# Performance work log

Hardware: AMD Instinct MI355X
Metric: run time of the kernel (lower is better)

The kernel has to match this reference:

```python
import jax, jax.numpy as jnp
import numpy as np

N_LAYER = 2


def setup_inputs() -> dict:
    key = jax.random.key(0)
    k1, k2, k3, k4, k5 = jax.random.split(key, 5)
    N, E, D, C = 50000, 800000, 128, 40
    features = jax.random.normal(k1, (N, D), dtype=jnp.float32)
    adj_row = jax.random.randint(k2, (E,), 0, N, dtype=jnp.int32)
    adj_col = jax.random.randint(k3, (E,), 0, N, dtype=jnp.int32)
    adj_values = jax.random.uniform(k4, (E,), dtype=jnp.float32)
    lin = jax.random.normal(k5, (D, C), dtype=jnp.float32) * (1.0 / np.sqrt(D))
    return {"features": features, "adj_row": adj_row, "adj_col": adj_col,
            "adj_values": adj_values, "lin": lin}


def reference(features, adj_row, adj_col, adj_values, lin):
    N = features.shape[0]
    loop = jnp.arange(N, dtype=adj_row.dtype)
    # preprocess_adj: add self-loops, symmetric GCN normalization D^-1/2 (A+I) D^-1/2
    row = jnp.concatenate([adj_row, loop])
    col = jnp.concatenate([adj_col, loop])
    val = jnp.concatenate([adj_values, jnp.ones((N,), features.dtype)])
    deg = jax.ops.segment_sum(val, row, num_segments=N)
    dinv = jnp.where(deg > 0, jax.lax.rsqrt(jnp.maximum(deg, 1e-12)), 0.0)
    nval = dinv[row] * val * dinv[col]  # normalized edge weights [E+N]
    X = features
    layerwise = []
    for _ in range(N_LAYER):  # X = A_hat @ X (SpMM via gather + segment_sum)
        X = jax.ops.segment_sum(nval[:, None] * X[col], row, num_segments=N)
        layerwise.append(X)
    logits = X @ lin  # [N, out_dim]
    return (jax.nn.log_softmax(logits, axis=1), logits, tuple(layerwise))
```

## Files before the change

kernel.cpp:

```cpp
#include <hip/hip_runtime.h>
#include <math.h>

#define D_FEAT 128
#define SCAN_B 256
#define C_MAX  40
#define FIXP   33554432.0f


__device__ __forceinline__ unsigned bf16_rne(float x) {
    unsigned u = __float_as_uint(x);
    return (u + 0x7fffu + ((u >> 16) & 1u)) >> 16;
}
__device__ __forceinline__ unsigned pack2(float x, float y) {
    return bf16_rne(x) | (bf16_rne(y) << 16);
}
__device__ __forceinline__ float lo_f(unsigned g) { return __uint_as_float(g << 16); }
__device__ __forceinline__ float hi_f(unsigned g) { return __uint_as_float(g & 0xffff0000u); }


__global__ void k_init(unsigned long long* __restrict__ deg64, int N) {
    int i = blockIdx.x * blockDim.x + threadIdx.x;
    if (i < N) deg64[i] = (unsigned long long)(1.0f * FIXP);
}

__global__ void k_deg_hist(const int* __restrict__ row, const float* __restrict__ val,
                           unsigned long long* __restrict__ deg64,
                           int* __restrict__ rank, int E) {
    int e = blockIdx.x * blockDim.x + threadIdx.x;
    if (e >= E) return;
    int r = row[e];
    unsigned long long add = (1ull << 40) |
                             (unsigned long long)(val[e] * FIXP + 0.5f);
    unsigned long long old = atomicAdd(&deg64[r], add);
    rank[e] = (int)(old >> 40);
}


__global__ __launch_bounds__(SCAN_B) void k_part_sum(const unsigned long long* __restrict__ deg64,
                                                     int* __restrict__ part,
                                                     float* __restrict__ dinv,
                                                     int* __restrict__ cnt32, int N) {
    __shared__ int s[SCAN_B];
    int i = blockIdx.x * SCAN_B + threadIdx.x;
    int c = 0;
    if (i < N) {
        unsigned long long p = deg64[i];
        int cntv = (int)(p >> 40);
        float deg = (float)(p & ((1ull << 40) - 1)) * (1.0f / FIXP);
        dinv[i] = rsqrtf(fmaxf(deg, 1e-12f));
        c = (cntv + 7) & ~7;
        cnt32[i] = c;
    }
    s[threadIdx.x] = c;
    __syncthreads();
    for (int off = SCAN_B / 2; off; off >>= 1) {
        if (threadIdx.x < off) s[threadIdx.x] += s[threadIdx.x + off];
        __syncthreads();
    }
    if (threadIdx.x == 0) part[blockIdx.x] = s[0];
}

__global__ __launch_bounds__(SCAN_B) void k_part_scan(int* __restrict__ part, int nchunks,
                                                      int* __restrict__ rowptr, int N) {
    __shared__ int s[SCAN_B];
    int t = threadIdx.x;
    int v = (t < nchunks) ? part[t] : 0;
    s[t] = v;
    __syncthreads();
    for (int off = 1; off < SCAN_B; off <<= 1) {
        int add = (t >= off) ? s[t - off] : 0;
        __syncthreads();
        s[t] += add;
        __syncthreads();
    }
    if (t < nchunks) part[t] = s[t] - v;
    if (t == nchunks - 1) rowptr[N] = s[t];
}

__global__ __launch_bounds__(SCAN_B) void k_chunk_scan(const int* __restrict__ cnt32,
                                                       const int* __restrict__ part,
                                                       int* __restrict__ rowptr, int N) {
    __shared__ int s[SCAN_B];
    int t = threadIdx.x;
    int i = blockIdx.x * SCAN_B + t;
    int v = (i < N) ? cnt32[i] : 0;
    s[t] = v;
    __syncthreads();
    for (int off = 1; off < SCAN_B; off <<= 1) {
        int add = (t >= off) ? s[t - off] : 0;
        __syncthreads();
        s[t] += add;
        __syncthreads();
    }
    if (i < N) rowptr[i] = part[blockIdx.x] + s[t] - v;
}

__global__ void k_convert(const float* __restrict__ X, const float* __restrict__ dinv,
                          unsigned* __restrict__ Xb, int N) {
    int t = blockIdx.x * blockDim.x + threadIdx.x;
    if (t >= N * (D_FEAT / 8)) return;
    float w = dinv[t >> 4];
    float4 a = ((const float4*)X)[t * 2];
    float4 b = ((const float4*)X)[t * 2 + 1];
    uint4 o;
    o.x = pack2(w * a.x, w * a.y); o.y = pack2(w * a.z, w * a.w);
    o.z = pack2(w * b.x, w * b.y); o.w = pack2(w * b.z, w * b.w);
    ((uint4*)Xb)[t] = o;
}

__global__ void k_scatter(const int* __restrict__ row, const int* __restrict__ col,
                          const float* __restrict__ val, const int* __restrict__ rank,
                          const int* __restrict__ rowptr, int2* __restrict__ csr, int E) {
    int e = blockIdx.x * blockDim.x + threadIdx.x;
    if (e >= E) return;
    int r = row[e];
    int pos = rowptr[r] + rank[e];
    csr[pos] = make_int2(col[e] << 8, __float_as_int(val[e]));
}


__device__ __forceinline__ float2 spmm_row_bf16(const int* __restrict__ rowptr,
                                                const int2* __restrict__ csr,
                                                const char* __restrict__ XbB,
                                                int rowi, int lane) {
    const unsigned lane4 = (unsigned)lane << 2;
    unsigned gs = *(const unsigned*)(XbB + ((unsigned)rowi << 8) + lane4);
    float2 a0 = make_float2(lo_f(gs), hi_f(gs));
    float2 a1 = make_float2(0.f, 0.f), a2 = make_float2(0.f, 0.f), a3 = make_float2(0.f, 0.f);
    int e  = rowptr[rowi];
    int e1 = rowptr[rowi + 1];

    for (; e + 16 <= e1; e += 16) {
        const int4* cp = (const int4*)(csr + e);
        int4 q0 = cp[0], q1 = cp[1], q2 = cp[2], q3 = cp[3];
        int4 q4 = cp[4], q5 = cp[5], q6 = cp[6], q7 = cp[7];
        unsigned g0 = *(const unsigned*)(XbB + (unsigned)q0.x + lane4);
        unsigned g1 = *(const unsigned*)(XbB + (unsigned)q0.z + lane4);
        unsigned g2 = *(const unsigned*)(XbB + (unsigned)q1.x + lane4);
        unsigned g3 = *(const unsigned*)(XbB + (unsigned)q1.z + lane4);
        unsigned g4 = *(const unsigned*)(XbB + (unsigned)q2.x + lane4);
        unsigned g5 = *(const unsigned*)(XbB + (unsigned)q2.z + lane4);
        unsigned g6 = *(const unsigned*)(XbB + (unsigned)q3.x + lane4);
        unsigned g7 = *(const unsigned*)(XbB + (unsigned)q3.z + lane4);
        unsigned g8 = *(const unsigned*)(XbB + (unsigned)q4.x + lane4);
        unsigned g9 = *(const unsigned*)(XbB + (unsigned)q4.z + lane4);
        unsigned ga = *(const unsigned*)(XbB + (unsigned)q5.x + lane4);
        unsigned gb = *(const unsigned*)(XbB + (unsigned)q5.z + lane4);
        unsigned gc = *(const unsigned*)(XbB + (unsigned)q6.x + lane4);
        unsigned gd = *(const unsigned*)(XbB + (unsigned)q6.z + lane4);
        unsigned ge = *(const unsigned*)(XbB + (unsigned)q7.x + lane4);
        unsigned gf = *(const unsigned*)(XbB + (unsigned)q7.z + lane4);
        float w0 = __int_as_float(q0.y), w1 = __int_as_float(q0.w);
        float w2 = __int_as_float(q1.y), w3 = __int_as_float(q1.w);
        float w4 = __int_as_float(q2.y), w5 = __int_as_float(q2.w);
        float w6 = __int_as_float(q3.y), w7 = __int_as_float(q3.w);
        float w8 = __int_as_float(q4.y), w9 = __int_as_float(q4.w);
        float wa = __int_as_float(q5.y), wb = __int_as_float(q5.w);
        float wc = __int_as_float(q6.y), wd = __int_as_float(q6.w);
        float we = __int_as_float(q7.y), wf = __int_as_float(q7.w);
        a0.x += w0 * lo_f(g0); a0.y += w0 * hi_f(g0);
        a1.x += w1 * lo_f(g1); a1.y += w1 * hi_f(g1);
        a2.x += w2 * lo_f(g2); a2.y += w2 * hi_f(g2);
        a3.x += w3 * lo_f(g3); a3.y += w3 * hi_f(g3);
        a0.x += w4 * lo_f(g4); a0.y += w4 * hi_f(g4);
        a1.x += w5 * lo_f(g5); a1.y += w5 * hi_f(g5);
        a2.x += w6 * lo_f(g6); a2.y += w6 * hi_f(g6);
        a3.x += w7 * lo_f(g7); a3.y += w7 * hi_f(g7);
        a0.x += w8 * lo_f(g8); a0.y += w8 * hi_f(g8);
        a1.x += w9 * lo_f(g9); a1.y += w9 * hi_f(g9);
        a2.x += wa * lo_f(ga); a2.y += wa * hi_f(ga);
        a3.x += wb * lo_f(gb); a3.y += wb * hi_f(gb);
        a0.x += wc * lo_f(gc); a0.y += wc * hi_f(gc);
        a1.x += wd * lo_f(gd); a1.y += wd * hi_f(gd);
        a2.x += we * lo_f(ge); a2.y += we * hi_f(ge);
        a3.x += wf * lo_f(gf); a3.y += wf * hi_f(gf);
    }
    if (e < e1) {
        const int4* cp = (const int4*)(csr + e);
        int4 q0 = cp[0], q1 = cp[1], q2 = cp[2], q3 = cp[3];
        unsigned g0 = *(const unsigned*)(XbB + (unsigned)q0.x + lane4);
        unsigned g1 = *(const unsigned*)(XbB + (unsigned)q0.z + lane4);
        unsigned g2 = *(const unsigned*)(XbB + (unsigned)q1.x + lane4);
        unsigned g3 = *(const unsigned*)(XbB + (unsigned)q1.z + lane4);
        unsigned g4 = *(const unsigned*)(XbB + (unsigned)q2.x + lane4);
        unsigned g5 = *(const unsigned*)(XbB + (unsigned)q2.z + lane4);
        unsigned g6 = *(const unsigned*)(XbB + (unsigned)q3.x + lane4);
        unsigned g7 = *(const unsigned*)(XbB + (unsigned)q3.z + lane4);
        float w0 = __int_as_float(q0.y), w1 = __int_as_float(q0.w);
        float w2 = __int_as_float(q1.y), w3 = __int_as_float(q1.w);
        float w4 = __int_as_float(q2.y), w5 = __int_as_float(q2.w);
        float w6 = __int_as_float(q3.y), w7 = __int_as_float(q3.w);
        a0.x += w0 * lo_f(g0); a0.y += w0 * hi_f(g0);
        a1.x += w1 * lo_f(g1); a1.y += w1 * hi_f(g1);
        a2.x += w2 * lo_f(g2); a2.y += w2 * hi_f(g2);
        a3.x += w3 * lo_f(g3); a3.y += w3 * hi_f(g3);
        a0.x += w4 * lo_f(g4); a0.y += w4 * hi_f(g4);
        a1.x += w5 * lo_f(g5); a1.y += w5 * hi_f(g5);
        a2.x += w6 * lo_f(g6); a2.y += w6 * hi_f(g6);
        a3.x += w7 * lo_f(g7); a3.y += w7 * hi_f(g7);
    }
    float2 acc;
    acc.x = (a0.x + a1.x) + (a2.x + a3.x);
    acc.y = (a0.y + a1.y) + (a2.y + a3.y);
    return acc;
}


__global__ __launch_bounds__(256) void k_spmm_l1(const int* __restrict__ rowptr,
                                                 const int2* __restrict__ csr,
                                                 const float* __restrict__ dinv,
                                                 const unsigned* __restrict__ Xb,
                                                 float* __restrict__ Xout,
                                                 unsigned* __restrict__ XbOut, int N) {
    int lane = threadIdx.x & 63;
    int wid  = threadIdx.x >> 6;
    int rowi = blockIdx.x * 4 + wid;
    if (rowi >= N) return;
    float2 acc = spmm_row_bf16(rowptr, csr, (const char*)Xb, rowi, lane);
    float dr = dinv[rowi];
    float2 x1 = make_float2(dr * acc.x, dr * acc.y);
    ((float2*)Xout)[(size_t)rowi * 64 + lane] = x1;
    XbOut[((unsigned)rowi << 6) | lane] = pack2(dr * x1.x, dr * x1.y);
}

__global__ __launch_bounds__(256) void k_spmm_l2_head(const int* __restrict__ rowptr,
                                                      const int2* __restrict__ csr,
                                                      const float* __restrict__ dinv,
                                                      const unsigned* __restrict__ Xb,
                                                      float* __restrict__ Xout,
                                                      const float* __restrict__ lin,
                                                      float* __restrict__ lsm,
                                                      float* __restrict__ logits,
                                                      int N, int C) {
    __shared__ float lin_s[D_FEAT * C_MAX];
    __shared__ float xs[4][D_FEAT];
    int lane = threadIdx.x & 63;
    int wid  = threadIdx.x >> 6;
    int rowi = blockIdx.x * 4 + wid;

    for (int i = threadIdx.x; i < D_FEAT * C; i += 256) lin_s[i] = lin[i];

    float2 x2 = make_float2(0.f, 0.f);
    if (rowi < N) {
        float2 acc = spmm_row_bf16(rowptr, csr, (const char*)Xb, rowi, lane);
        float dr = dinv[rowi];
        x2 = make_float2(dr * acc.x, dr * acc.y);
        ((float2*)Xout)[(size_t)rowi * 64 + lane] = x2;
        xs[wid][2 * lane]     = x2.x;
        xs[wid][2 * lane + 1] = x2.y;
    }
    __syncthreads();
    if (rowi >= N) return;

    float a = 0.0f;
    if (lane < C) {
#pragma unroll 8
        for (int d = 0; d < D_FEAT; ++d)
            a += xs[wid][d] * lin_s[d * C + lane];
    }
    float m = (lane < C) ? a : -INFINITY;
    for (int off = 32; off; off >>= 1) m = fmaxf(m, __shfl_xor(m, off));
    float ev = (lane < C) ? __expf(a - m) : 0.0f;
    float s = ev;
    for (int off = 32; off; off >>= 1) s += __shfl_xor(s, off);
    float lse = m + logf(s);
    if (lane < C) {
        logits[(size_t)rowi * C + lane] = a;
        lsm[(size_t)rowi * C + lane]    = a - lse;
    }
}


__global__ __launch_bounds__(256) void k_spmm_f32(const int* __restrict__ rowptr,
                                                  const int2* __restrict__ csr,
                                                  const float* __restrict__ dinv,
                                                  const float* __restrict__ Xin,
                                                  float* __restrict__ Xout, int N) {
    int lane = threadIdx.x & 63;
    int wid  = threadIdx.x >> 6;
    int rowi = blockIdx.x * 4 + wid;
    if (rowi >= N) return;
    const float2* Xin2 = (const float2*)Xin;
    float dr = dinv[rowi];
    float2 v0 = Xin2[(size_t)rowi * 64 + lane];
    float2 a0 = make_float2(dr * v0.x, dr * v0.y);
    float2 a1 = make_float2(0.f, 0.f);
    int e  = rowptr[rowi];
    int e1 = rowptr[rowi + 1];
    for (; e < e1; e += 2) {
        int2 q0 = csr[e], q1 = csr[e + 1];
        unsigned c0 = (unsigned)q0.x >> 8, c1 = (unsigned)q1.x >> 8;
        float w0 = __int_as_float(q0.y) * dinv[c0];
        float w1 = __int_as_float(q1.y) * dinv[c1];
        float2 g0 = Xin2[(size_t)c0 * 64 + lane];
        float2 g1 = Xin2[(size_t)c1 * 64 + lane];
        a0.x += w0 * g0.x; a0.y += w0 * g0.y;
        a1.x += w1 * g1.x; a1.y += w1 * g1.y;
    }
    float2 acc = make_float2(dr * (a0.x + a1.x), dr * (a0.y + a1.y));
    ((float2*)Xout)[(size_t)rowi * 64 + lane] = acc;
}

__global__ __launch_bounds__(256) void k_head(const float* __restrict__ X,
                                              const float* __restrict__ lin,
                                              float* __restrict__ lsm,
                                              float* __restrict__ logits,
                                              int N, int C) {
    __shared__ float xs[4][D_FEAT];
    int lane = threadIdx.x & 63;
    int wid  = threadIdx.x >> 6;
    int node = blockIdx.x * 4 + wid;
    if (node < N) {
        xs[wid][lane]      = X[(size_t)node * D_FEAT + lane];
        xs[wid][lane + 64] = X[(size_t)node * D_FEAT + 64 + lane];
    }
    __syncthreads();
    if (node >= N) return;

    float acc = 0.0f;
    if (lane < C) {
        for (int d = 0; d < D_FEAT; ++d)
            acc += xs[wid][d] * lin[d * C + lane];
    }
    float m = (lane < C) ? acc : -INFINITY;
    for (int off = 32; off; off >>= 1) m = fmaxf(m, __shfl_xor(m, off));
    float ev = (lane < C) ? __expf(acc - m) : 0.0f;
    float s = ev;
    for (int off = 32; off; off >>= 1) s += __shfl_xor(s, off);
    float lse = m + logf(s);
    if (lane < C) {
        logits[(size_t)node * C + lane] = acc;
        lsm[(size_t)node * C + lane]    = acc - lse;
    }
}


extern "C" void kernel_launch(void* const* d_in, const int* in_sizes, int n_in,
                              void* d_out, int out_size, void* d_ws, size_t ws_size,
                              hipStream_t stream) {
    const float* features = (const float*)d_in[0];
    const int*   adj_row  = (const int*)d_in[1];
    const int*   adj_col  = (const int*)d_in[2];
    const float* adj_val  = (const float*)d_in[3];
    const float* lin      = (const float*)d_in[4];

    const int N = in_sizes[0] / D_FEAT;
    const int E = in_sizes[1];
    const int C = in_sizes[4] / D_FEAT;
    const int csrTot = E + 8 * N;

    float* out = (float*)d_out;
    const size_t NC = (size_t)N * C;
    const size_t ND = (size_t)N * D_FEAT;
    float* lsm    = out;
    float* logits = out + NC;
    float* X1     = out + 2 * NC;
    float* X2     = out + 2 * NC + ND;

    char* wp = (char*)d_ws;
    auto alloc = [&](size_t bytes) { char* p = wp; wp += (bytes + 15) & ~(size_t)15; return p; };
    unsigned long long* deg64 = (unsigned long long*)alloc((size_t)N * 8);
    float*    dinv   = (float*)alloc((size_t)N * 4);
    int*      cnt32  = (int*)alloc((size_t)N * 4);
    int*      rowptr = (int*)alloc((size_t)(N + 1) * 4);
    int*      part   = (int*)alloc(256 * 4);
    int*      rank   = (int*)alloc((size_t)E * 4);
    int2*     csr    = (int2*)alloc((size_t)csrTot * 8);
    unsigned* Xb0    = (unsigned*)alloc((size_t)N * (D_FEAT / 2) * 4);
    unsigned* Xb1    = (unsigned*)alloc((size_t)N * (D_FEAT / 2) * 4);

    const bool bf16_ok = ((size_t)(wp - (char*)d_ws) <= ws_size) && (C <= C_MAX);

    const int B = 256;
    const int nchunks = (N + SCAN_B - 1) / SCAN_B;

    hipMemsetAsync(csr, 0, (size_t)csrTot * 8, stream);
    k_init<<<(N + B - 1) / B, B, 0, stream>>>(deg64, N);
    k_deg_hist<<<(E + B - 1) / B, B, 0, stream>>>(adj_row, adj_val, deg64, rank, E);
    k_part_sum<<<nchunks, SCAN_B, 0, stream>>>(deg64, part, dinv, cnt32, N);
    k_part_scan<<<1, SCAN_B, 0, stream>>>(part, nchunks, rowptr, N);
    k_chunk_scan<<<nchunks, SCAN_B, 0, stream>>>(cnt32, part, rowptr, N);
    k_scatter<<<(E + B - 1) / B, B, 0, stream>>>(adj_row, adj_col, adj_val, rank,
                                                 rowptr, csr, E);

    int spmmBlocks = (N + 3) / 4;
    if (bf16_ok) {
        k_convert<<<(N * (D_FEAT / 8) + B - 1) / B, B, 0, stream>>>(features, dinv, Xb0, N);
        k_spmm_l1<<<spmmBlocks, 256, 0, stream>>>(rowptr, csr, dinv, Xb0, X1, Xb1, N);
        k_spmm_l2_head<<<spmmBlocks, 256, 0, stream>>>(rowptr, csr, dinv, Xb1, X2,
                                                       lin, lsm, logits, N, C);
    } else {
        k_spmm_f32<<<spmmBlocks, 256, 0, stream>>>(rowptr, csr, dinv, features, X1, N);
        k_spmm_f32<<<spmmBlocks, 256, 0, stream>>>(rowptr, csr, dinv, X1, X2, N);
        k_head<<<(N + 3) / 4, 256, 0, stream>>>(X2, lin, lsm, logits, N, C);
    }
}
```

Measured before the change: 181.7 us.

## Fuse three-pass scan into decoupled-lookback scan and merge scatter with convert

Replaces the partial-sum, partition-scan and chunk-scan kernels with a single kernel that uses a ticket-ordered decoupled lookback to build rowptr. The full CSR memset is dropped; only the padding slots of each row are zeroed inside the scan kernel. The edge scatter and the bf16 feature conversion are merged into one launch. This cuts several kernel launches and a large memset, at the cost of serialized spin-waits on chunk state across blocks.

```diff
diff --git a/kernel.cpp b/kernel.cpp
--- a/kernel.cpp
+++ b/kernel.cpp
@@ -6,6 +6,9 @@
 #define C_MAX  40
 #define FIXP   33554432.0f
 
+#define FLAG_AGG (1ull << 32)
+#define FLAG_INC (2ull << 32)
+
 
 __device__ __forceinline__ unsigned bf16_rne(float x) {
     unsigned u = __float_as_uint(x);
@@ -18,9 +21,14 @@
 __device__ __forceinline__ float hi_f(unsigned g) { return __uint_as_float(g & 0xffff0000u); }
 
 
-__global__ void k_init(unsigned long long* __restrict__ deg64, int N) {
+__global__ void k_init(unsigned long long* __restrict__ deg64,
+                       unsigned* __restrict__ ticket,
+                       unsigned long long* __restrict__ chunkState,
+                       int N, int nchunks) {
     int i = blockIdx.x * blockDim.x + threadIdx.x;
     if (i < N) deg64[i] = (unsigned long long)(1.0f * FIXP);
+    if (i < nchunks) chunkState[i] = 0ull;
+    if (i == 0) *ticket = 0u;
 }
 
 __global__ void k_deg_hist(const int* __restrict__ row, const float* __restrict__ val,
@@ -36,36 +44,30 @@
 }
 
 
-__global__ __launch_bounds__(SCAN_B) void k_part_sum(const unsigned long long* __restrict__ deg64,
-                                                     int* __restrict__ part,
+__global__ __launch_bounds__(SCAN_B) void k_scan_all(const unsigned long long* __restrict__ deg64,
                                                      float* __restrict__ dinv,
-                                                     int* __restrict__ cnt32, int N) {
+                                                     int* __restrict__ rowptr,
+                                                     int2* __restrict__ csr,
+                                                     unsigned* __restrict__ ticket,
+                                                     unsigned long long* __restrict__ chunkState,
+                                                     int N, int nchunks) {
     __shared__ int s[SCAN_B];
-    int i = blockIdx.x * SCAN_B + threadIdx.x;
-    int c = 0;
+    __shared__ int vc_s, exc_s;
+    int t = threadIdx.x;
+    if (t == 0) vc_s = (int)atomicAdd(ticket, 1u);
+    __syncthreads();
+    int vc = vc_s;
+    int i = vc * SCAN_B + t;
+
+    int cr = 0, c = 0;
     if (i < N) {
         unsigned long long p = deg64[i];
-        int cntv = (int)(p >> 40);
+        cr = (int)(p >> 40);
         float deg = (float)(p & ((1ull << 40) - 1)) * (1.0f / FIXP);
         dinv[i] = rsqrtf(fmaxf(deg, 1e-12f));
-        c = (cntv + 7) & ~7;
-        cnt32[i] = c;
-    }
-    s[threadIdx.x] = c;
-    __syncthreads();
-    for (int off = SCAN_B / 2; off; off >>= 1) {
-        if (threadIdx.x < off) s[threadIdx.x] += s[threadIdx.x + off];
-        __syncthreads();
-    }
-    if (threadIdx.x == 0) part[blockIdx.x] = s[0];
-}
-
-__global__ __launch_bounds__(SCAN_B) void k_part_scan(int* __restrict__ part, int nchunks,
-                                                      int* __restrict__ rowptr, int N) {
-    __shared__ int s[SCAN_B];
-    int t = threadIdx.x;
-    int v = (t < nchunks) ? part[t] : 0;
-    s[t] = v;
+        c = (cr + 7) & ~7;
+    }
+    s[t] = c;
     __syncthreads();
     for (int off = 1; off < SCAN_B; off <<= 1) {
         int add = (t >= off) ? s[t - off] : 0;
@@ -73,39 +75,61 @@
         s[t] += add;
         __syncthreads();
     }
-    if (t < nchunks) part[t] = s[t] - v;
-    if (t == nchunks - 1) rowptr[N] = s[t];
-}
-
-__global__ __launch_bounds__(SCAN_B) void k_chunk_scan(const int* __restrict__ cnt32,
-                                                       const int* __restrict__ part,
-                                                       int* __restrict__ rowptr, int N) {
-    __shared__ int s[SCAN_B];
-    int t = threadIdx.x;
-    int i = blockIdx.x * SCAN_B + t;
-    int v = (i < N) ? cnt32[i] : 0;
-    s[t] = v;
+    int incl = s[t];
+    int blockSum = s[SCAN_B - 1];
+
+    if (t == 0) {
+        int exc = 0;
+        if (vc == 0) {
+            atomicExch(&chunkState[0], FLAG_INC | (unsigned long long)(unsigned)blockSum);
+        } else {
+            atomicExch(&chunkState[vc], FLAG_AGG | (unsigned long long)(unsigned)blockSum);
+            int j = vc - 1;
+            int acc = 0;
+            for (;;) {
+                unsigned long long st;
+                do { st = atomicAdd(&chunkState[j], 0ull); } while ((st >> 32) == 0);
+                acc += (int)(st & 0xffffffffull);
+                if (st & FLAG_INC) break;
+                --j;
+            }
+            exc = acc;
+            atomicExch(&chunkState[vc], FLAG_INC | (unsigned long long)(unsigned)(acc + blockSum));
+        }
+        exc_s = exc;
+    }
     __syncthreads();
-    for (int off = 1; off < SCAN_B; off <<= 1) {
-        int add = (t >= off) ? s[t - off] : 0;
-        __syncthreads();
-        s[t] += add;
-        __syncthreads();
-    }
-    if (i < N) rowptr[i] = part[blockIdx.x] + s[t] - v;
-}
-
-__global__ void k_convert(const float* __restrict__ X, const float* __restrict__ dinv,
-                          unsigned* __restrict__ Xb, int N) {
+    int base = exc_s;
+
+    if (i < N) {
+        int rp = base + incl - c;
+        rowptr[i] = rp;
+        for (int k = cr; k < c; ++k) csr[rp + k] = make_int2(0, 0);
+    }
+    if (vc == nchunks - 1 && t == SCAN_B - 1) rowptr[N] = base + incl;
+}
+
+__global__ void k_scatter_convert(const int* __restrict__ row, const int* __restrict__ col,
+                                  const float* __restrict__ val, const int* __restrict__ rank,
+                                  const int* __restrict__ rowptr, int2* __restrict__ csr,
+                                  const float* __restrict__ X, const float* __restrict__ dinv,
+                                  unsigned* __restrict__ Xb, int E, int NV) {
     int t = blockIdx.x * blockDim.x + threadIdx.x;
-    if (t >= N * (D_FEAT / 8)) return;
-    float w = dinv[t >> 4];
-    float4 a = ((const float4*)X)[t * 2];
-    float4 b = ((const float4*)X)[t * 2 + 1];
-    uint4 o;
-    o.x = pack2(w * a.x, w * a.y); o.y = pack2(w * a.z, w * a.w);
-    o.z = pack2(w * b.x, w * b.y); o.w = pack2(w * b.z, w * b.w);
-    ((uint4*)Xb)[t] = o;
+    if (t < E) {
+        int r = row[t];
+        csr[rowptr[r] + rank[t]] = make_int2(col[t] << 8, __float_as_int(val[t]));
+    } else {
+        int u = t - E;
+        if (u < NV) {
+            float w = dinv[u >> 4];
+            float4 a = ((const float4*)X)[u * 2];
+            float4 b = ((const float4*)X)[u * 2 + 1];
+            uint4 o;
+            o.x = pack2(w * a.x, w * a.y); o.y = pack2(w * a.z, w * a.w);
+            o.z = pack2(w * b.x, w * b.y); o.w = pack2(w * b.z, w * b.w);
+            ((uint4*)Xb)[u] = o;
+        }
+    }
 }
 
 __global__ void k_scatter(const int* __restrict__ row, const int* __restrict__ col,
@@ -114,8 +138,7 @@
     int e = blockIdx.x * blockDim.x + threadIdx.x;
     if (e >= E) return;
     int r = row[e];
-    int pos = rowptr[r] + rank[e];
-    csr[pos] = make_int2(col[e] << 8, __float_as_int(val[e]));
+    csr[rowptr[r] + rank[e]] = make_int2(col[e] << 8, __float_as_int(val[e]));
 }
 
 
@@ -240,11 +263,10 @@
 
     for (int i = threadIdx.x; i < D_FEAT * C; i += 256) lin_s[i] = lin[i];
 
-    float2 x2 = make_float2(0.f, 0.f);
     if (rowi < N) {
         float2 acc = spmm_row_bf16(rowptr, csr, (const char*)Xb, rowi, lane);
         float dr = dinv[rowi];
-        x2 = make_float2(dr * acc.x, dr * acc.y);
+        float2 x2 = make_float2(dr * acc.x, dr * acc.y);
         ((float2*)Xout)[(size_t)rowi * 64 + lane] = x2;
         xs[wid][2 * lane]     = x2.x;
         xs[wid][2 * lane + 1] = x2.y;
@@ -348,6 +370,7 @@
     const int E = in_sizes[1];
     const int C = in_sizes[4] / D_FEAT;
     const int csrTot = E + 8 * N;
+    const int nchunks = (N + SCAN_B - 1) / SCAN_B;
 
     float* out = (float*)d_out;
     const size_t NC = (size_t)N * C;
@@ -359,37 +382,38 @@
 
     char* wp = (char*)d_ws;
     auto alloc = [&](size_t bytes) { char* p = wp; wp += (bytes + 15) & ~(size_t)15; return p; };
-    unsigned long long* deg64 = (unsigned long long*)alloc((size_t)N * 8);
-    float*    dinv   = (float*)alloc((size_t)N * 4);
-    int*      cnt32  = (int*)alloc((size_t)N * 4);
-    int*      rowptr = (int*)alloc((size_t)(N + 1) * 4);
-    int*      part   = (int*)alloc(256 * 4);
-    int*      rank   = (int*)alloc((size_t)E * 4);
-    int2*     csr    = (int2*)alloc((size_t)csrTot * 8);
-    unsigned* Xb0    = (unsigned*)alloc((size_t)N * (D_FEAT / 2) * 4);
-    unsigned* Xb1    = (unsigned*)alloc((size_t)N * (D_FEAT / 2) * 4);
+    unsigned long long* deg64      = (unsigned long long*)alloc((size_t)N * 8);
+    float*              dinv       = (float*)alloc((size_t)N * 4);
+    int*                rowptr     = (int*)alloc((size_t)(N + 1) * 4);
+    unsigned*           ticket     = (unsigned*)alloc(16);
+    unsigned long long* chunkState = (unsigned long long*)alloc((size_t)nchunks * 8);
+    int*                rank       = (int*)alloc((size_t)E * 4);
+    int2*               csr        = (int2*)alloc((size_t)csrTot * 8);
+    unsigned*           Xb0        = (unsigned*)alloc((size_t)N * (D_FEAT / 2) * 4);
+    unsigned*           Xb1        = (unsigned*)alloc((size_t)N * (D_FEAT / 2) * 4);
 
     const bool bf16_ok = ((size_t)(wp - (char*)d_ws) <= ws_size) && (C <= C_MAX);
 
     const int B = 256;
-    const int nchunks = (N + SCAN_B - 1) / SCAN_B;
-
-    hipMemsetAsync(csr, 0, (size_t)csrTot * 8, stream);
-    k_init<<<(N + B - 1) / B, B, 0, stream>>>(deg64, N);
+
+    k_init<<<(N + B - 1) / B, B, 0, stream>>>(deg64, ticket, chunkState, N, nchunks);
     k_deg_hist<<<(E + B - 1) / B, B, 0, stream>>>(adj_row, adj_val, deg64, rank, E);
-    k_part_sum<<<nchunks, SCAN_B, 0, stream>>>(deg64, part, dinv, cnt32, N);
-    k_part_scan<<<1, SCAN_B, 0, stream>>>(part, nchunks, rowptr, N);
-    k_chunk_scan<<<nchunks, SCAN_B, 0, stream>>>(cnt32, part, rowptr, N);
-    k_scatter<<<(E + B - 1) / B, B, 0, stream>>>(adj_row, adj_col, adj_val, rank,
-                                                 rowptr, csr, E);
-
-    int spmmBlocks = (N + 3) / 4;
+    k_scan_all<<<nchunks, SCAN_B, 0, stream>>>(deg64, dinv, rowptr, csr,
+                                               ticket, chunkState, N, nchunks);
+
     if (bf16_ok) {
-        k_convert<<<(N * (D_FEAT / 8) + B - 1) / B, B, 0, stream>>>(features, dinv, Xb0, N);
+        const int NV = N * (D_FEAT / 8);
+        k_scatter_convert<<<(E + NV + B - 1) / B, B, 0, stream>>>(adj_row, adj_col, adj_val,
+                                                                  rank, rowptr, csr,
+                                                                  features, dinv, Xb0, E, NV);
+        int spmmBlocks = (N + 3) / 4;
         k_spmm_l1<<<spmmBlocks, 256, 0, stream>>>(rowptr, csr, dinv, Xb0, X1, Xb1, N);
         k_spmm_l2_head<<<spmmBlocks, 256, 0, stream>>>(rowptr, csr, dinv, Xb1, X2,
                                                        lin, lsm, logits, N, C);
     } else {
+        k_scatter<<<(E + B - 1) / B, B, 0, stream>>>(adj_row, adj_col, adj_val, rank,
+                                                     rowptr, csr, E);
+        int spmmBlocks = (N + 3) / 4;
         k_spmm_f32<<<spmmBlocks, 256, 0, stream>>>(rowptr, csr, dinv, features, X1, N);
         k_spmm_f32<<<spmmBlocks, 256, 0, stream>>>(rowptr, csr, dinv, X1, X2, N);
         k_head<<<(N + 3) / 4, 256, 0, stream>>>(X2, lin, lsm, logits, N, C);
```

New measurement: 181.0 us (median of 2 runs). Within noise of the previous version (-0.4%).
